# Kernel tuning notes

Hardware: AMD Instinct MI355X
Metric: run time of the kernel (lower is better)

Reference implementation:

```python
import jax, jax.numpy as jnp
import numpy as np
from jax import lax

GAMMA = 1.0  # init gamma


def setup_inputs() -> dict:
    key = jax.random.key(0)
    k = jax.random.split(key, 6)
    B, T1, T2, D, WD = 64, 320, 320, 768, 32
    x = jax.random.normal(k[0], (B, T1, D), jnp.float32)
    y = jax.random.normal(k[1], (B, T2, D), jnp.float32)
    # nn.Linear(input_dim, warp_dim): weight [WD, D], bias [WD]
    W = jax.random.normal(k[2], (WD, D), jnp.float32) / np.sqrt(D).astype(np.float32)
    b = 0.01 * jax.random.normal(k[3], (WD,), jnp.float32)
    warp_scale = 1.0 + 0.1 * jax.random.normal(k[4], (WD,), jnp.float32)
    warp_shift = 0.1 * jax.random.normal(k[5], (WD,), jnp.float32)
    return {"x": x, "y": y, "W": W, "b": b, "warp_scale": warp_scale, "warp_shift": warp_shift}


def _soft_dtw_path(xw, yw, gamma):
    # Faithful banded soft-DTW DP: cells outside the band stay 0 and ARE read
    # by in-band neighbors, exactly as the torch loop does.
    B, T1, _ = xw.shape
    T2 = yw.shape[1]
    bw = max(T1, T2) // 4 + 1
    # squared euclidean distances [B,T1,T2] (expanded form to avoid B*T1*T2*D blow-up)
    x2 = jnp.sum(xw * xw, -1)[:, :, None]
    y2 = jnp.sum(yw * yw, -1)[:, None, :]
    dist = x2 + y2 - 2.0 * jnp.einsum('bid,bjd->bij', xw, yw)
    NEG = jnp.float32(-1e30)  # disables a candidate inside logsumexp
    t2s = jnp.arange(T2)

    def outer(prev_row, xs):  # prev_row: path[t1-1, :] of shape [B,T2]
        t1, drow = xs  # drow: dist[:, t1, :] -> [B,T2]
        diag_prev = jnp.concatenate([jnp.zeros((B, 1), drow.dtype), prev_row[:, :-1]], axis=1)

        def inner(left, ins):  # left: path[t1, t2-1] -> [B]
            t2, d, up, diag = ins
            z = jnp.stack([
                jnp.where((t1 > 0) & (t2 > 0), -diag / gamma, NEG),
                jnp.where(t1 > 0, -up / gamma, NEG),
                jnp.where(t2 > 0, -left / gamma, NEG),
            ], axis=0)  # [3,B]
            softmin = -gamma * jax.nn.logsumexp(z, axis=0)
            val = d + jnp.where((t1 > 0) | (t2 > 0), softmin, 0.0)
            in_band = (t2 >= t1 - bw) & (t2 <= t1 + bw - 1)
            val = jnp.where(in_band, val, 0.0)
            return val, val

        _, row = lax.scan(inner, jnp.zeros((B,), drow.dtype),
                          (t2s, drow.T, prev_row.T, diag_prev.T))
        row = row.T  # [B,T2]
        return row, row

    _, path = lax.scan(outer, jnp.zeros((B, T2), dist.dtype),
                       (jnp.arange(T1), jnp.transpose(dist, (1, 0, 2))))
    path = jnp.transpose(path, (1, 0, 2))  # [B,T1,T2]
    return jax.nn.softmax(-path / gamma, axis=-1)


def reference(x, y, W, b, warp_scale, warp_shift):
    xw = (x @ W.T + b) * warp_scale + warp_shift
    yw = (y @ W.T + b) * warp_scale + warp_shift
    path = _soft_dtw_path(xw, yw, GAMMA)  # [B,T1,T2] softmax probs
    pn = path / (jnp.sum(path, axis=1, keepdims=True) + 1e-10)
    aligned = jnp.einsum('bts,btd->bsd', pn, x)  # bmm(path^T, x) -> [B,T2,D]
    return aligned, path
```

## Files before the change

kernel.cpp:

```cpp
#include <hip/hip_runtime.h>

#define NB 64
#define T 320
#define D 768
#define WD 32
#define NSTEP 639
#define NBLK 80
#define BSTRIDE (NBLK * 1024)
#define BIG 1e30f
#define LOG2E 1.44269504088896340736f
#define LN2 0.69314718055994530942f

__device__ __forceinline__ float dpp_ror1(float v) {
  return __int_as_float(__builtin_amdgcn_update_dpp(
      0, __float_as_int(v), 0x13C, 0xF, 0xF, true));
}
__device__ __forceinline__ float dpp_rol1(float v) {
  return __int_as_float(__builtin_amdgcn_update_dpp(
      0, __float_as_int(v), 0x134, 0xF, 0xF, true));
}

__global__ __launch_bounds__(256) void prep_kernel(
    const float* __restrict__ W, const float* __restrict__ bias,
    const float* __restrict__ wscale, const float* __restrict__ wshift,
    float* __restrict__ WeT, float* __restrict__ beff) {
  int i = blockIdx.x * 256 + threadIdx.x;
  int c = i >> 5, k = i & 31;
  WeT[i] = W[k * D + c] * wscale[k];
  if (i < WD) beff[i] = bias[i] * wscale[i] + wshift[i];
}

__global__ __launch_bounds__(256) void proj_kernel(
    const float* __restrict__ x, const float* __restrict__ y,
    const float* __restrict__ WeT, const float* __restrict__ beff,
    float* __restrict__ xw, float* __restrict__ yw) {
  __shared__ float lds[8448];
  int tid = threadIdx.x;
  int w = tid >> 6, l = tid & 63;
  int rbase = blockIdx.x * 64;
  float acc[32];
#pragma unroll
  for (int k = 0; k < 32; ++k) acc[k] = 0.f;
#pragma clang loop unroll(disable)
  for (int ch = 0; ch < 6; ++ch) {
    __syncthreads();
#pragma unroll
    for (int p = 0; p < 8; ++p) {
      int idx = p * 256 + tid;
      int row = idx >> 5;
      int c4 = idx & 31;
      int r = rbase + row;
      const float* src = (r < NB * T) ? x + (size_t)r * D
                                      : y + (size_t)(r - NB * T) * D;
      float4 v = *(const float4*)(src + ch * 128 + c4 * 4);
      lds[row * 129 + c4 * 4 + 0] = v.x;
      lds[row * 129 + c4 * 4 + 1] = v.y;
      lds[row * 129 + c4 * 4 + 2] = v.z;
      lds[row * 129 + c4 * 4 + 3] = v.w;
    }
    __syncthreads();
    int woff = __builtin_amdgcn_readfirstlane((ch * 128 + w * 32) * 32);
    const float* wp = WeT + woff;
#pragma unroll
    for (int cc = 0; cc < 32; ++cc) {
      float xv = lds[l * 129 + w * 32 + cc];
#pragma unroll
      for (int k = 0; k < 32; ++k)
        acc[k] = fmaf(wp[cc * 32 + k], xv, acc[k]);
    }
  }
  __syncthreads();
#pragma unroll
  for (int k = 0; k < 32; ++k) lds[w * 2112 + l * 33 + k] = acc[k];
  __syncthreads();
  int idx = tid * 8;
  int row = idx >> 5;
  int k0 = idx & 31;
  float o[8];
#pragma unroll
  for (int e = 0; e < 8; ++e)
    o[e] = lds[0 * 2112 + row * 33 + k0 + e] + lds[1 * 2112 + row * 33 + k0 + e] +
           lds[2 * 2112 + row * 33 + k0 + e] + lds[3 * 2112 + row * 33 + k0 + e] +
           beff[k0 + e];
  int rr = rbase + row;
  float* dst = (rr < NB * T) ? xw + (size_t)rr * WD + k0
                             : yw + (size_t)(rr - NB * T) * WD + k0;
  float4 o0 = {o[0], o[1], o[2], o[3]}, o1 = {o[4], o[5], o[6], o[7]};
  *(float4*)dst = o0;
  *(float4*)(dst + 4) = o1;
}

__global__ __launch_bounds__(256) void dist_kernel(
    const float* __restrict__ xw, const float* __restrict__ yw,
    float* __restrict__ dc) {
  int b = blockIdx.y;
  int i = blockIdx.x * 256 + threadIdx.x;
  int dblk = i >> 10;
  int a = (i >> 3) & 127;
  int k = i & 7;
  if (a >= 81) return;
  int d = dblk * 8 + k;
  if (d >= NSTEP) return;
  int par = (d + 1) & 1;
  int base = (d + 81 - par) >> 1;
  int t1 = base - a;
  int t2 = d - t1;
  if ((unsigned)t1 >= (unsigned)T || (unsigned)t2 >= (unsigned)T) return;
  const float4* xr = (const float4*)(xw + ((size_t)b * T + t1) * WD);
  const float4* yr = (const float4*)(yw + ((size_t)b * T + t2) * WD);
  float s = 0.f;
#pragma unroll
  for (int q = 0; q < 8; ++q) {
    float4 xv = xr[q], yv = yr[q];
    float d0 = xv.x - yv.x, d1 = xv.y - yv.y, d2 = xv.z - yv.z, d3 = xv.w - yv.w;
    s = fmaf(d0, d0, s); s = fmaf(d1, d1, s); s = fmaf(d2, d2, s); s = fmaf(d3, d3, s);
  }
  dc[(size_t)b * BSTRIDE + i] = s * LOG2E;
}

#define FSTEP(DP_, DS_, PAR, DVAL)                                             \
  {                                                                            \
    const int d_ = (DVAL);                                                     \
    const int base_ = (d_ + 81 - (PAR)) >> 1;                                  \
    float shP, shS;                                                            \
    if (PAR) { shP = dpp_rol1((l == 0) ? v0b : v0); shS = dpp_rol1(v0b); }     \
    else     { shP = dpp_ror1(v1); shS = dpp_ror1((l == 63) ? v1 : v1b); }     \
    int t1 = base_ - l, t2 = d_ - t1;                                          \
    {                                                                          \
      bool valid = ((unsigned)t1 < (unsigned)T) && ((unsigned)t2 < (unsigned)T); \
      float up, left, diag;                                                    \
      if (PAR) { left = v0; up = shP; diag = v1; }                             \
      else     { up = v1; left = (l == 0) ? 0.f : shP; diag = v0; }            \
      float cu = (t1 > 0) ? up : BIG;                                          \
      float cl = (t2 > 0) ? left : BIG;                                        \
      float cd = (t1 > 0 && t2 > 0) ? diag : BIG;                              \
      float mn = fminf(fminf(cu, cl), cd);                                     \
      float mx = fmaxf(fmaxf(cu, cl), cd);                                     \
      float md = fmaxf(fminf(cu, cl), fminf(fmaxf(cu, cl), cd));               \
      float ss = 1.f + __builtin_amdgcn_exp2f(mn - md) +                       \
                 __builtin_amdgcn_exp2f(mn - mx);                              \
      float val = (DP_) + mn - __builtin_amdgcn_logf(ss);                      \
      if ((DVAL) == 0) val = (DP_);                                            \
      if (valid) {                                                             \
        if (PAR) v1 = val; else v0 = val;                                      \
        outb[t1 * T + t2] = val * LN2;                                         \
      }                                                                        \
    }                                                                          \
    {                                                                          \
      int t1b = t1 - 64, t2b = t2 + 64;                                        \
      bool valid = (l < 17) && ((unsigned)t1b < (unsigned)T) &&                \
                   ((unsigned)t2b < (unsigned)T);                              \
      float up, left, diag;                                                    \
      if (PAR) { left = v0b; up = (l == 16) ? 0.f : shS; diag = v1b; }         \
      else     { up = v1b; left = shS; diag = v0b; }                           \
      float cu = (t1b > 0) ? up : BIG;                                         \
      float cl = (t2b > 0) ? left : BIG;                                       \
      float cd = (t1b > 0 && t2b > 0) ? diag : BIG;                            \
      float mn = fminf(fminf(cu, cl), cd);                                     \
      float mx = fmaxf(fmaxf(cu, cl), cd);                                     \
      float md = fmaxf(fminf(cu, cl), fminf(fmaxf(cu, cl), cd));               \
      float ss = 1.f + __builtin_amdgcn_exp2f(mn - md) +                       \
                 __builtin_amdgcn_exp2f(mn - mx);                              \
      float val = (DS_) + mn - __builtin_amdgcn_logf(ss);                      \
      if (valid) {                                                             \
        if (PAR) v1b = val; else v0b = val;                                    \
        outb[t1b * T + t2b] = val * LN2;                                       \
      }                                                                        \
    }                                                                          \
  }

#define SSTEP(DP_, DS_, PAR, IOFF)                                             \
  {                                                                            \
    float shP, shS;                                                            \
    if (PAR) { shP = dpp_rol1((l == 0) ? v0b : v0); shS = dpp_rol1(v0b); }     \
    else     { shP = dpp_ror1(v1); shS = dpp_ror1((l == 63) ? v1 : v1b); }     \
    {                                                                          \
      float up, left, diag;                                                    \
      if (PAR) { left = v0; up = shP; diag = v1; }                             \
      else     { up = v1; left = (l == 0) ? 0.f : shP; diag = v0; }            \
      float mn = fminf(fminf(up, left), diag);                                 \
      float mx = fmaxf(fmaxf(up, left), diag);                                 \
      float md = fmaxf(fminf(up, left), fminf(fmaxf(up, left), diag));         \
      float ss = 1.f + __builtin_amdgcn_exp2f(mn - md) +                       \
                 __builtin_amdgcn_exp2f(mn - mx);                              \
      float val = (DP_) + mn - __builtin_amdgcn_logf(ss);                      \
      if (PAR) v1 = val; else v0 = val;                                        \
      outb[io + (IOFF)] = val * LN2;                                           \
    }                                                                          \
    {                                                                          \
      float up, left, diag;                                                    \
      if (PAR) { left = v0b; up = (l == 16) ? 0.f : shS; diag = v1b; }         \
      else     { up = v1b; left = shS; diag = v0b; }                           \
      float mn = fminf(fminf(up, left), diag);                                 \
      float mx = fmaxf(fmaxf(up, left), diag);                                 \
      float md = fmaxf(fminf(up, left), fminf(fmaxf(up, left), diag));         \
      float ss = 1.f + __builtin_amdgcn_exp2f(mn - md) +                       \
                 __builtin_amdgcn_exp2f(mn - mx);                              \
      float val = (DS_) + mn - __builtin_amdgcn_logf(ss);                      \
      if (PAR) v1b = val; else v0b = val;                                      \
      if (l < 17) outb[ioS + (IOFF)] = val * LN2;                              \
    }                                                                          \
  }

#define LOADBLK(R0, R1, S0v, S1v, DBLK)                                        \
  {                                                                            \
    const float4* q_ = (const float4*)(dcb + (DBLK) * 1024 + l * 8);           \
    R0 = q_[0]; R1 = q_[1];                                                    \
    const float4* q2_ = (const float4*)(dcb + (DBLK) * 1024 + (64 + l) * 8);   \
    S0v = q2_[0]; S1v = q2_[1];                                                \
  }

#define BLK8_F(P0, P1, S0v, S1v, DB)                                           \
  FSTEP(P0.x, S0v.x, 1, (DB) + 0) FSTEP(P0.y, S0v.y, 0, (DB) + 1)              \
  FSTEP(P0.z, S0v.z, 1, (DB) + 2) FSTEP(P0.w, S0v.w, 0, (DB) + 3)              \
  FSTEP(P1.x, S1v.x, 1, (DB) + 4) FSTEP(P1.y, S1v.y, 0, (DB) + 5)              \
  FSTEP(P1.z, S1v.z, 1, (DB) + 6) FSTEP(P1.w, S1v.w, 0, (DB) + 7)

#define BLK8_S(P0, P1, S0v, S1v)                                               \
  SSTEP(P0.x, S0v.x, 1, 0)   SSTEP(P0.y, S0v.y, 0, 320)                        \
  SSTEP(P0.z, S0v.z, 1, 321) SSTEP(P0.w, S0v.w, 0, 641)                        \
  io += 642; ioS += 642;                                                       \
  SSTEP(P1.x, S1v.x, 1, 0)   SSTEP(P1.y, S1v.y, 0, 320)                        \
  SSTEP(P1.z, S1v.z, 1, 321) SSTEP(P1.w, S1v.w, 0, 641)                        \
  io += 642; ioS += 642;

__global__ __launch_bounds__(64) void dtw_kernel(
    const float* __restrict__ dc, float* __restrict__ path) {
  int b = blockIdx.x;
  int l = threadIdx.x;
  const float* dcb = dc + (size_t)b * BSTRIDE;
  float* outb = path + (size_t)b * T * T;
  float v0 = 0.f, v1 = 0.f, v0b = 0.f, v1b = 0.f;
  float4 aP0, aP1, aS0, aS1, bP0, bP1, bS0, bS1;
  int io = 0, ioS = 0;

  if (l == 40) {
    float d00 = dcb[320];
    v1 = d00;
    outb[0] = d00 * LN2;
  }
  LOADBLK(aP0, aP1, aS0, aS1, 0)
#pragma clang loop unroll(disable)
  for (int it = 0; it < 6; ++it) {
    int dbase = it * 16;
    int blk = it * 2;
    LOADBLK(bP0, bP1, bS0, bS1, blk + 1)
    BLK8_F(aP0, aP1, aS0, aS1, dbase)
    LOADBLK(aP0, aP1, aS0, aS1, blk + 2)
    BLK8_F(bP0, bP1, bS0, bS1, dbase + 8)
  }
  io = 28168 - 319 * l;
  ioS = io - 20416;
#pragma clang loop unroll(disable)
  for (int it = 0; it < 27; ++it) {
    int blk = 12 + it * 2;
    LOADBLK(bP0, bP1, bS0, bS1, blk + 1)
    BLK8_S(aP0, aP1, aS0, aS1)
    LOADBLK(aP0, aP1, aS0, aS1, blk + 2)
    BLK8_S(bP0, bP1, bS0, bS1)
  }
#pragma clang loop unroll(disable)
  for (int it = 0; it < 6; ++it) {
    int dbase = 528 + it * 16;
    int blk = 66 + it * 2;
    LOADBLK(bP0, bP1, bS0, bS1, blk + 1)
    BLK8_F(aP0, aP1, aS0, aS1, dbase)
    LOADBLK(aP0, aP1, aS0, aS1, blk + 2)
    BLK8_F(bP0, bP1, bS0, bS1, dbase + 8)
  }
  LOADBLK(bP0, bP1, bS0, bS1, 79)
  BLK8_F(aP0, aP1, aS0, aS1, 624)
  FSTEP(bP0.x, bS0.x, 1, 632) FSTEP(bP0.y, bS0.y, 0, 633)
  FSTEP(bP0.z, bS0.z, 1, 634) FSTEP(bP0.w, bS0.w, 0, 635)
  FSTEP(bP1.x, bS1.x, 1, 636) FSTEP(bP1.y, bS1.y, 0, 637)
  FSTEP(bP1.z, bS1.z, 1, 638)
}

__global__ __launch_bounds__(T) void softmax_kernel(float* __restrict__ path,
                                                    float* __restrict__ cvec) {
  __shared__ float sm1[5], sm2[5];
  int row = blockIdx.x;
  int t1 = row % T;
  int j = threadIdx.x;
  float* p = path + (size_t)row * T;
  bool in = (j >= t1 - 81) && (j <= t1 + 80);
  float v = in ? p[j] : 0.f;
  float m = v;
#pragma unroll
  for (int off = 32; off >= 1; off >>= 1) m = fminf(m, __shfl_xor(m, off, 64));
  int w = j >> 6;
  if ((j & 63) == 0) sm1[w] = m;
  __syncthreads();
  m = fminf(fminf(fminf(sm1[0], sm1[1]), fminf(sm1[2], sm1[3])), sm1[4]);
  float e = __expf(m - v);
  float s = e;
#pragma unroll
  for (int off = 32; off >= 1; off >>= 1) s += __shfl_xor(s, off, 64);
  if ((j & 63) == 0) sm2[w] = s;
  __syncthreads();
  s = sm2[0] + sm2[1] + sm2[2] + sm2[3] + sm2[4];
  p[j] = e / s;
  if (j == 0) cvec[row] = __expf(m - 0.f) / s;
}

__global__ __launch_bounds__(256) void gk_kernel(
    const float* __restrict__ x, const float* __restrict__ cvec,
    float* __restrict__ g) {
  int b = blockIdx.y;
  int d0 = blockIdx.x * 256 + threadIdx.x;
  const float* xb = x + (size_t)b * T * D + d0;
  const float* cb = cvec + b * T;
  float s = 0.f;
  for (int t = 0; t < T; ++t) s = fmaf(cb[t], xb[(size_t)t * D], s);
  g[b * D + d0] = s;
}

__global__ __launch_bounds__(256) void colsum_kernel(
    const float* __restrict__ path, const float* __restrict__ cvec,
    float* __restrict__ scale) {
  __shared__ float red[4][64];
  __shared__ float cbred[4];
  int b = blockIdx.y;
  int tid = threadIdx.x;
  int l = tid & 63, tq = tid >> 6;
  int j = blockIdx.x * 64 + l;
  const float* cb = cvec + b * T;
  float c = cb[tid];
  if (tid < 64) c += cb[256 + tid];
#pragma unroll
  for (int off = 32; off >= 1; off >>= 1) c += __shfl_xor(c, off, 64);
  if (l == 0) cbred[tq] = c;
  float s = 0.f;
  int t0 = j - 80 + tq * 41;
  const float* p = path + (size_t)b * T * T + j;
#pragma unroll 4
  for (int i = 0; i < 41; ++i) {
    int t = t0 + i;
    if ((unsigned)t < (unsigned)T) s += p[(size_t)t * T] - cb[t];
  }
  red[tq][l] = s;
  __syncthreads();
  if (tq == 0) {
    float cs = red[0][l] + red[1][l] + red[2][l] + red[3][l] +
               (cbred[0] + cbred[1] + cbred[2] + cbred[3]);
    scale[b * T + j] = 1.f / (cs + 1e-10f);
  }
}

#define TSB 64
#define TDB 256
#define TKB 16
__global__ __launch_bounds__(256) void bmm_kernel(
    const float* __restrict__ path, const float* __restrict__ x,
    const float* __restrict__ cvec, const float* __restrict__ g,
    const float* __restrict__ scale, float* __restrict__ out) {
  __shared__ __align__(16) float Pl[TKB][TSB];
  __shared__ __align__(16) float Xl[TKB][TDB];
  int bid = blockIdx.x;
  int wgid = (bid & 7) * 120 + (bid >> 3);
  int b = wgid / 15;
  int r = wgid - b * 15;
  int s0 = (r / 3) * TSB;
  int d0 = (r % 3) * TDB;
  int tid = threadIdx.x;
  int ts = tid & 7, td = tid >> 3;
  const float* pb = path + (size_t)b * T * T;
  const float* xb = x + (size_t)b * T * D;
  const float* cb = cvec + b * T;
  float acc[8][8];
  {
    const float* gb = g + b * D + d0 + td * 8;
    float4 g0 = *(const float4*)gb;
    float4 g1 = *(const float4*)(gb + 4);
    float gv[8] = {g0.x, g0.y, g0.z, g0.w, g1.x, g1.y, g1.z, g1.w};
#pragma unroll
    for (int i = 0; i < 8; ++i)
#pragma unroll
      for (int jj = 0; jj < 8; ++jj) acc[i][jj] = gv[jj];
  }
  int t_lo = s0 - 80; if (t_lo < 0) t_lo = 0; t_lo &= ~15;
  int t_hi = (s0 + 160) & ~15; if (t_hi > T) t_hi = T;
  for (int t0 = t_lo; t0 < t_hi; t0 += TKB) {
    __syncthreads();
    {
      int tr = tid >> 4, sc = (tid & 15) * 4;
      float4 p4 = *(const float4*)&pb[(size_t)(t0 + tr) * T + s0 + sc];
      float cv = cb[t0 + tr];
      p4.x -= cv; p4.y -= cv; p4.z -= cv; p4.w -= cv;
      *(float4*)&Pl[tr][sc] = p4;
    }
    {
      int tr = tid >> 4, c0 = (tid & 15) * 4;
#pragma unroll
      for (int q = 0; q < 4; ++q)
        *(float4*)&Xl[tr][c0 + q * 64] =
            *(const float4*)&xb[(size_t)(t0 + tr) * D + d0 + c0 + q * 64];
    }
    __syncthreads();
#pragma unroll
    for (int t = 0; t < TKB; ++t) {
      float4 pa = *(const float4*)&Pl[t][ts * 8];
      float4 pc = *(const float4*)&Pl[t][ts * 8 + 4];
      float4 xa = *(const float4*)&Xl[t][td * 8];
      float4 xc = *(const float4*)&Xl[t][td * 8 + 4];
      float pv[8] = {pa.x, pa.y, pa.z, pa.w, pc.x, pc.y, pc.z, pc.w};
      float xv[8] = {xa.x, xa.y, xa.z, xa.w, xc.x, xc.y, xc.z, xc.w};
#pragma unroll
      for (int i = 0; i < 8; ++i)
#pragma unroll
        for (int jj = 0; jj < 8; ++jj)
          acc[i][jj] = fmaf(pv[i], xv[jj], acc[i][jj]);
    }
  }
#pragma unroll
  for (int i = 0; i < 8; ++i) {
    int s = s0 + ts * 8 + i;
    float sc = scale[b * T + s];
    float* op = out + ((size_t)b * T + s) * D + d0 + td * 8;
    float4 o0, o1;
    o0.x = acc[i][0] * sc; o0.y = acc[i][1] * sc; o0.z = acc[i][2] * sc; o0.w = acc[i][3] * sc;
    o1.x = acc[i][4] * sc; o1.y = acc[i][5] * sc; o1.z = acc[i][6] * sc; o1.w = acc[i][7] * sc;
    *(float4*)op = o0;
    *(float4*)(op + 4) = o1;
  }
}

extern "C" void kernel_launch(void* const* d_in, const int* in_sizes, int n_in,
                              void* d_out, int out_size, void* d_ws, size_t ws_size,
                              hipStream_t stream) {
  const float* x = (const float*)d_in[0];
  const float* y = (const float*)d_in[1];
  const float* W = (const float*)d_in[2];
  const float* bias = (const float*)d_in[3];
  const float* wscale = (const float*)d_in[4];
  const float* wshift = (const float*)d_in[5];
  float* outp = (float*)d_out;
  float* aligned = outp;
  float* path = outp + (size_t)NB * T * D;
  float* distc = aligned;
  float* ws = (float*)d_ws;
  float* xw = ws;
  float* yw = xw + (size_t)NB * T * WD;
  float* scale = yw + (size_t)NB * T * WD;
  float* WeT = scale + (size_t)NB * T;
  float* beff = WeT + (size_t)WD * D;
  float* cvec = beff + WD;
  float* g = cvec + (size_t)NB * T;

  prep_kernel<<<dim3((WD * D) / 256), 256, 0, stream>>>(W, bias, wscale, wshift, WeT, beff);
  proj_kernel<<<dim3((2 * NB * T) / 64), 256, 0, stream>>>(x, y, WeT, beff, xw, yw);
  dist_kernel<<<dim3(BSTRIDE / 256, NB), 256, 0, stream>>>(xw, yw, distc);
  dtw_kernel<<<dim3(NB), 64, 0, stream>>>(distc, path);
  softmax_kernel<<<dim3(NB * T), T, 0, stream>>>(path, cvec);
  gk_kernel<<<dim3(D / 256, NB), 256, 0, stream>>>(x, cvec, g);
  colsum_kernel<<<dim3(T / 64, NB), 256, 0, stream>>>(path, cvec, scale);
  bmm_kernel<<<dim3((D / TDB) * (T / TSB) * NB), 256, 0, stream>>>(path, x, cvec, g, scale, aligned);
}
```

Measured before the change: 378.8 us.

## Tile banded distance kernel through LDS with 4x4 register blocking

The distance kernel no longer has each thread compute one diagonal-ordered cell by reading full xw/yw rows from global memory. Each block now stages a 64-row tile of xw and a 64-row tile of yw in shared memory. Each thread computes a 4x4 block of squared distances, and only in-band cells are scattered into the diagonal-major layout. This removes redundant global row loads at the cost of uncoalesced scattered stores and some wasted compute on out-of-band cells in the tiles.

```diff
diff --git a/kernel.cpp b/kernel.cpp
--- a/kernel.cpp
+++ b/kernel.cpp
@@ -93,29 +93,69 @@
 __global__ __launch_bounds__(256) void dist_kernel(
     const float* __restrict__ xw, const float* __restrict__ yw,
     float* __restrict__ dc) {
+  __shared__ float xs[64][33];
+  __shared__ float ys[64][33];
   int b = blockIdx.y;
-  int i = blockIdx.x * 256 + threadIdx.x;
-  int dblk = i >> 10;
-  int a = (i >> 3) & 127;
-  int k = i & 7;
-  if (a >= 81) return;
-  int d = dblk * 8 + k;
-  if (d >= NSTEP) return;
-  int par = (d + 1) & 1;
-  int base = (d + 81 - par) >> 1;
-  int t1 = base - a;
-  int t2 = d - t1;
-  if ((unsigned)t1 >= (unsigned)T || (unsigned)t2 >= (unsigned)T) return;
-  const float4* xr = (const float4*)(xw + ((size_t)b * T + t1) * WD);
-  const float4* yr = (const float4*)(yw + ((size_t)b * T + t2) * WD);
-  float s = 0.f;
-#pragma unroll
-  for (int q = 0; q < 8; ++q) {
-    float4 xv = xr[q], yv = yr[q];
-    float d0 = xv.x - yv.x, d1 = xv.y - yv.y, d2 = xv.z - yv.z, d3 = xv.w - yv.w;
-    s = fmaf(d0, d0, s); s = fmaf(d1, d1, s); s = fmaf(d2, d2, s); s = fmaf(d3, d3, s);
-  }
-  dc[(size_t)b * BSTRIDE + i] = s * LOG2E;
+  int cidx = blockIdx.x;
+  int t1c = (cidx >> 2) * 64;
+  int t2c = t1c - 88 + (cidx & 3) * 64;
+  int tid = threadIdx.x;
+  {
+    int r = tid >> 2, c4 = tid & 3;
+    const float* sx = xw + ((size_t)b * T + t1c + r) * WD;
+    *(float4*)&xs[r][c4 * 4] = *(const float4*)(sx + c4 * 4);
+    *(float4*)&xs[r][(c4 + 4) * 4] = *(const float4*)(sx + (c4 + 4) * 4);
+    int t2r = t2c + r;
+    if ((unsigned)t2r < (unsigned)T) {
+      const float* sy = yw + ((size_t)b * T + t2r) * WD;
+      *(float4*)&ys[r][c4 * 4] = *(const float4*)(sy + c4 * 4);
+      *(float4*)&ys[r][(c4 + 4) * 4] = *(const float4*)(sy + (c4 + 4) * 4);
+    }
+  }
+  __syncthreads();
+  int ts1 = (tid >> 4) * 4;
+  int ts2 = (tid & 15) * 4;
+  float acc[4][4];
+#pragma unroll
+  for (int i = 0; i < 4; ++i)
+#pragma unroll
+    for (int j = 0; j < 4; ++j) acc[i][j] = 0.f;
+#pragma unroll
+  for (int c4 = 0; c4 < 8; ++c4) {
+    float4 xv[4], yv[4];
+#pragma unroll
+    for (int i = 0; i < 4; ++i) xv[i] = *(const float4*)&xs[ts1 + i][c4 * 4];
+#pragma unroll
+    for (int j = 0; j < 4; ++j) yv[j] = *(const float4*)&ys[ts2 + j][c4 * 4];
+#pragma unroll
+    for (int i = 0; i < 4; ++i)
+#pragma unroll
+      for (int j = 0; j < 4; ++j) {
+        float d0 = xv[i].x - yv[j].x, d1 = xv[i].y - yv[j].y;
+        float d2 = xv[i].z - yv[j].z, d3 = xv[i].w - yv[j].w;
+        float s = acc[i][j];
+        s = fmaf(d0, d0, s); s = fmaf(d1, d1, s);
+        s = fmaf(d2, d2, s); s = fmaf(d3, d3, s);
+        acc[i][j] = s;
+      }
+  }
+  float* dcb = dc + (size_t)b * BSTRIDE;
+#pragma unroll
+  for (int i = 0; i < 4; ++i) {
+#pragma unroll
+    for (int j = 0; j < 4; ++j) {
+      int t1 = t1c + ts1 + i;
+      int t2 = t2c + ts2 + j;
+      int dt = t2 - t1;
+      if ((unsigned)t2 < (unsigned)T && dt >= -81 && dt <= 80) {
+        int d = t1 + t2;
+        int par = (d + 1) & 1;
+        int base = (d + 81 - par) >> 1;
+        int a = base - t1;
+        dcb[((d >> 3) << 10) + (a << 3) + (d & 7)] = acc[i][j] * LOG2E;
+      }
+    }
+  }
 }
 
 #define FSTEP(DP_, DS_, PAR, DVAL)                                             \
@@ -449,7 +489,7 @@
 
   prep_kernel<<<dim3((WD * D) / 256), 256, 0, stream>>>(W, bias, wscale, wshift, WeT, beff);
   proj_kernel<<<dim3((2 * NB * T) / 64), 256, 0, stream>>>(x, y, WeT, beff, xw, yw);
-  dist_kernel<<<dim3(BSTRIDE / 256, NB), 256, 0, stream>>>(xw, yw, distc);
+  dist_kernel<<<dim3(20, NB), 256, 0, stream>>>(xw, yw, distc);
   dtw_kernel<<<dim3(NB), 64, 0, stream>>>(distc, path);
   softmax_kernel<<<dim3(NB * T), T, 0, stream>>>(path, cvec);
   gk_kernel<<<dim3(D / 256, NB), 256, 0, stream>>>(x, cvec, g);
```

Result: faster. 326.5 us (-13.8%).
